# Kernel optimization log

Measured on AMD Instinct MI355X. Metric: run time of the kernel, lower is better.

## Reference

```python
import jax, jax.numpy as jnp
import numpy as np

NL, H, PD, NH, NB = 4, 256, 64, 4, 65
B, L, AA = 2, 384, 48
DH = H // NH
MAX_REL = 32


def _ln(x, g, b):
    m = x.mean(-1, keepdims=True)
    v = ((x - m) ** 2).mean(-1, keepdims=True)
    return (x - m) * jax.lax.rsqrt(v + 1e-5) * g + b


def setup_inputs() -> dict:
    key = jax.random.key(0)
    ks = iter(jax.random.split(key, 64))
    w = lambda *s: jax.random.normal(next(ks), s, jnp.float32) * 0.02
    return dict(
        x=jax.random.normal(next(ks), (B, L, AA), jnp.float32),
        rp_w=w(AA, H), rp_b=jnp.zeros((H,), jnp.float32),
        pos_embed=w(L, H),
        pii_w=w(H, PD), pii_b=jnp.zeros((PD,), jnp.float32),
        pij_w=w(H, PD), pij_b=jnp.zeros((PD,), jnp.float32),
        rel_emb=w(2 * MAX_REL + 2, PD),
        ln_seq_g=jnp.ones((NL, H), jnp.float32), ln_seq_b=jnp.zeros((NL, H), jnp.float32),
        ln_pair_g=jnp.ones((NL, PD), jnp.float32), ln_pair_b=jnp.zeros((NL, PD), jnp.float32),
        pb_w=w(NL, PD, NH),
        in_w=w(NL, H, 3 * H), in_b=jnp.zeros((NL, 3 * H), jnp.float32),
        out_w=w(NL, H, H), out_b=jnp.zeros((NL, H), jnp.float32),
        ff_ln_g=jnp.ones((NL, H), jnp.float32), ff_ln_b=jnp.zeros((NL, H), jnp.float32),
        ff_w1=w(NL, H, 4 * H), ff_b1=jnp.zeros((NL, 4 * H), jnp.float32),
        ff_w2=w(NL, 4 * H, H), ff_b2=jnp.zeros((NL, H), jnp.float32),
        pu_ln_g=jnp.ones((NL, PD), jnp.float32), pu_ln_b=jnp.zeros((NL, PD), jnp.float32),
        pu_w1=w(NL, PD, PD), pu_b1=jnp.zeros((NL, PD), jnp.float32),
        pu_w2=w(NL, PD, PD), pu_b2=jnp.zeros((NL, PD), jnp.float32),
        outer_w=w(NL, 2 * H, PD), outer_b=jnp.zeros((NL, PD), jnp.float32),
        dh_ln_g=jnp.ones((PD,), jnp.float32), dh_ln_b=jnp.zeros((PD,), jnp.float32),
        dh_w1=w(PD, PD), dh_b1=jnp.zeros((PD,), jnp.float32),
        dh_w2=w(PD, NB), dh_b2=jnp.zeros((NB,), jnp.float32),
    )


def reference(x, rp_w, rp_b, pos_embed, pii_w, pii_b, pij_w, pij_b, rel_emb,
              ln_seq_g, ln_seq_b, ln_pair_g, ln_pair_b, pb_w, in_w, in_b,
              out_w, out_b, ff_ln_g, ff_ln_b, ff_w1, ff_b1, ff_w2, ff_b2,
              pu_ln_g, pu_ln_b, pu_w1, pu_b1, pu_w2, pu_b2, outer_w, outer_b,
              dh_ln_g, dh_ln_b, dh_w1, dh_b1, dh_w2, dh_b2):
    Bx, Lx, _ = x.shape
    gelu = lambda t: jax.nn.gelu(t, approximate=False)  # torch nn.GELU default (erf)
    h = x @ rp_w + rp_b + pos_embed[:Lx][None]
    # pair init: outer sum of two linear projections + clipped rel-pos embedding
    pair = (h @ pii_w + pii_b)[:, :, None, :] + (h @ pij_w + pij_b)[:, None, :, :]
    idx = jnp.arange(Lx)
    rel = jnp.clip(idx[None, :] - idx[:, None], -MAX_REL, MAX_REL) + MAX_REL  # (L,L)
    pair = pair + rel_emb[rel][None]
    for i in range(NL):
        seq_n = _ln(h, ln_seq_g[i], ln_seq_b[i])
        bias = _ln(pair, ln_pair_g[i], ln_pair_b[i]) @ pb_w[i]  # (B,L,L,NH)
        mask = bias.mean(axis=(0, 3))  # torch: permute->reshape(B*NH,L,L)->mean(0)
        qkv = seq_n @ in_w[i] + in_b[i]
        q, k, v = jnp.split(qkv, 3, axis=-1)
        q = q.reshape(Bx, Lx, NH, DH)
        k = k.reshape(Bx, Lx, NH, DH)
        v = v.reshape(Bx, Lx, NH, DH)
        scores = jnp.einsum('blhd,bmhd->bhlm', q, k) / float(np.sqrt(DH)) + mask
        attn = jax.nn.softmax(scores, axis=-1)
        o = jnp.einsum('bhlm,bmhd->blhd', attn, v).reshape(Bx, Lx, H)
        h = h + o @ out_w[i] + out_b[i]
        h = h + gelu(_ln(h, ff_ln_g[i], ff_ln_b[i]) @ ff_w1[i] + ff_b1[i]) @ ff_w2[i] + ff_b2[i]
        # outer_proj(cat([h_i, h_j])) == h@W[:H] outer-summed with h@W[H:]
        oi = h @ outer_w[i][:H]
        oj = h @ outer_w[i][H:]
        outer = oi[:, :, None, :] + oj[:, None, :, :] + outer_b[i]  # (B,L,L,PD)
        pair = pair + gelu(_ln(outer, pu_ln_g[i], pu_ln_b[i]) @ pu_w1[i] + pu_b1[i]) @ pu_w2[i] + pu_b2[i]
    logits = gelu(_ln(pair, dh_ln_g, dh_ln_b) @ dh_w1 + dh_b1) @ dh_w2 + dh_b2
    return (logits + jnp.swapaxes(logits, 1, 2)) / 2.0
```

## Files before the change

### kernel.cpp

```cpp
#include <hip/hip_runtime.h>
#include <math.h>

#define LSEQ 384
#define HD 256
#define PDIM 64
#define NHEAD 4
#define NBINS 65
#define BATCH 2
#define NTT (LSEQ / 16)
#define NTRI (NTT * (NTT + 1) / 2)

typedef __attribute__((ext_vector_type(8))) short bf16x8;
typedef __attribute__((ext_vector_type(16))) float f32x16;
#define MFMA32(a, b, c) __builtin_amdgcn_mfma_f32_32x32x16_bf16(a, b, c, 0, 0, 0)

template<int CTRL, int RMASK>
__device__ __forceinline__ float dpp_sum_step(float v) {
    int x = __builtin_amdgcn_update_dpp(0, __float_as_int(v), CTRL, RMASK, 0xf, true);
    return v + __int_as_float(x);
}
template<int CTRL, int RMASK>
__device__ __forceinline__ float dpp_max_step(float v) {
    int x = __builtin_amdgcn_update_dpp(__float_as_int(v), __float_as_int(v), CTRL, RMASK, 0xf, false);
    return fmaxf(v, __int_as_float(x));
}
__device__ __forceinline__ float wsum(float v) {
    v = dpp_sum_step<0x111, 0xf>(v);
    v = dpp_sum_step<0x112, 0xf>(v);
    v = dpp_sum_step<0x114, 0xf>(v);
    v = dpp_sum_step<0x118, 0xf>(v);
    v = dpp_sum_step<0x142, 0xa>(v);
    v = dpp_sum_step<0x143, 0xc>(v);
    return __int_as_float(__builtin_amdgcn_readlane(__float_as_int(v), 63));
}
__device__ __forceinline__ float wmax(float v) {
    v = dpp_max_step<0x111, 0xf>(v);
    v = dpp_max_step<0x112, 0xf>(v);
    v = dpp_max_step<0x114, 0xf>(v);
    v = dpp_max_step<0x118, 0xf>(v);
    v = dpp_max_step<0x142, 0xa>(v);
    v = dpp_max_step<0x143, 0xc>(v);
    return __int_as_float(__builtin_amdgcn_readlane(__float_as_int(v), 63));
}
__device__ __forceinline__ float gelu_erf(float x) {
    return 0.5f * x * (1.0f + erff(x * 0.70710678f));
}

__device__ __forceinline__ unsigned short f2bf(float x) {
    unsigned u = __float_as_uint(x);
    unsigned r = (u + 0x7fff + ((u >> 16) & 1)) >> 16;
    return (unsigned short)r;
}
__device__ __forceinline__ float bf2f(unsigned short h) {
    return __uint_as_float(((unsigned)h) << 16);
}
__device__ __forceinline__ void split_bf(float x, unsigned short& h, unsigned short& l) {
    h = f2bf(x);
    l = f2bf(x - bf2f(h));
}

__global__ void k_h_init(const float* __restrict__ x, const float* __restrict__ rp_w,
                         const float* __restrict__ rp_b, const float* __restrict__ pos,
                         float* __restrict__ h) {
    __shared__ float xs[48];
    int row = blockIdx.x;
    int l = row % LSEQ;
    int t = threadIdx.x;
    if (t < 48) xs[t] = x[row * 48 + t];
    __syncthreads();
    float acc = rp_b[t] + pos[l * HD + t];
#pragma unroll 8
    for (int a = 0; a < 48; ++a) acc += xs[a] * rp_w[a * HD + t];
    h[row * HD + t] = acc;
}

__global__ void k_proj2(const float* __restrict__ h, const float* __restrict__ wA,
                        const float* __restrict__ wB, const float* __restrict__ bA,
                        const float* __restrict__ bB, int center,
                        float* __restrict__ pA, float* __restrict__ pB) {
    __shared__ float hs[HD];
    int row = blockIdx.x;
    int t = threadIdx.x;
    hs[t] = h[row * HD + t];
    hs[t + 128] = h[row * HD + t + 128];
    __syncthreads();
    int col = t & 63;
    const float* w = (t < 64) ? wA : wB;
    const float* bias = (t < 64) ? bA : bB;
    float acc = bias ? bias[col] : 0.0f;
#pragma unroll 8
    for (int a = 0; a < HD; ++a) acc += hs[a] * w[a * PDIM + col];
    if (center) {
        float mean = wsum(acc) * (1.0f / PDIM);
        acc -= mean;
    }
    float* p = (t < 64) ? pA : pB;
    p[row * PDIM + col] = acc;
}

__global__ void __launch_bounds__(64) k_pair_init2(
    const float* __restrict__ pi, const float* __restrict__ pj,
    const float* __restrict__ rel_emb, const float* __restrict__ gpb,
    const float* __restrict__ cbv, float* __restrict__ pair,
    float* __restrict__ mask_out) {
    __shared__ __align__(16) float pt[32][65];
    int blk = blockIdx.x;
    int row = blk / 12, seg = blk % 12;
    int b = row / LSEQ, i = row % LSEQ;
    int t = threadIdx.x;
    int pl = t & 31, hq = t >> 5;
    int j0 = seg * 32;
    float piv = pi[row * 64 + t];
    const float* pjb = pj + ((size_t)b * LSEQ + j0) * 64;
#pragma unroll 8
    for (int j = 0; j < 32; ++j) {
        int r = j0 + j - i; r = r < -32 ? -32 : (r > 32 ? 32 : r); r += 32;
        pt[j][t] = piv + pjb[j * 64 + t] + rel_emb[r * 64 + t];
    }
    __syncthreads();
    float4* dst4 = (float4*)(pair + ((size_t)row * LSEQ + j0) * 64);
    for (int n = t; n < 512; n += 64) {
        int r2 = n >> 4, c4 = (n & 15) << 2;
        float4 g4 = { pt[r2][c4], pt[r2][c4 + 1], pt[r2][c4 + 2], pt[r2][c4 + 3] };
        dst4[n] = g4;
    }
    float vv[32];
    float sv = 0.0f;
#pragma unroll
    for (int c = 0; c < 32; ++c) { vv[c] = pt[pl][hq * 32 + c]; sv += vv[c]; }
    sv += __shfl_xor(sv, 32);
    float mean = sv * (1.0f / PDIM);
    float sd2 = 0.0f, sdg = 0.0f;
#pragma unroll
    for (int c = 0; c < 32; ++c) {
        float d = vv[c] - mean;
        sd2 = fmaf(d, d, sd2);
        sdg = fmaf(d, gpb[hq * 32 + c], sdg);
    }
    sd2 += __shfl_xor(sd2, 32);
    sdg += __shfl_xor(sdg, 32);
    float rsv = rsqrtf(sd2 * (1.0f / PDIM) + 1e-5f);
    float dot = rsv * sdg + cbv[0];
    if (hq == 0)
        atomicAdd(mask_out + i * LSEQ + j0 + pl, dot * (1.0f / (BATCH * NHEAD)));
}

__global__ void k_prep(const float* __restrict__ pu_ln_g, const float* __restrict__ pu_ln_b,
                       const float* __restrict__ pu_w1, const float* __restrict__ pu_b1,
                       const float* __restrict__ pu_w2,
                       const float* __restrict__ dh_ln_g, const float* __restrict__ dh_ln_b,
                       const float* __restrict__ dh_w1, const float* __restrict__ dh_b1,
                       const float* __restrict__ dh_w2,
                       unsigned short* __restrict__ w1hT, unsigned short* __restrict__ w1lT,
                       unsigned short* __restrict__ w2hT, unsigned short* __restrict__ w2lT,
                       float* __restrict__ b1p, float* __restrict__ w2c) {
    int i = blockIdx.x;
    int c = threadIdx.x;
    const float *g, *bb, *w1, *b1, *w2;
    int w2s;
    if (i < 4) { g = pu_ln_g + i * 64; bb = pu_ln_b + i * 64; w1 = pu_w1 + i * 4096;
                 b1 = pu_b1 + i * 64; w2 = pu_w2 + i * 4096; w2s = 64; }
    else       { g = dh_ln_g; bb = dh_ln_b; w1 = dh_w1; b1 = dh_b1; w2 = dh_w2; w2s = 65; }
    float accb = b1[c];
    for (int k = 0; k < 64; ++k) {
        float wv = w1[k * 64 + c];
        accb += bb[k] * wv;
        unsigned short h, l;
        split_bf(g[k] * wv, h, l);
        w1hT[i * 4096 + c * 64 + k] = h;
        w1lT[i * 4096 + c * 64 + k] = l;
        split_bf(w2[k * w2s + c], h, l);
        w2hT[i * 4096 + c * 64 + k] = h;
        w2lT[i * 4096 + c * 64 + k] = l;
    }
    b1p[i * 64 + c] = accb;
    if (i == 4) w2c[c] = dh_w2[c * 65 + 64];
}

__global__ void k_maskprep(const float* __restrict__ g, const float* __restrict__ bb,
                           const float* __restrict__ pbw, float* __restrict__ gp,
                           float* __restrict__ cb) {
    int li = blockIdx.x;
    int c = threadIdx.x;
    const float* pw = pbw + li * PDIM * NHEAD;
    float pbs = pw[c * 4] + pw[c * 4 + 1] + pw[c * 4 + 2] + pw[c * 4 + 3];
    gp[li * 64 + c] = g[li * 64 + c] * pbs;
    float s = wsum(bb[li * 64 + c] * pbs);
    if (c == 0) cb[li] = s;
}

__global__ void k_split_T(const float* __restrict__ src, unsigned short* __restrict__ dh,
                          unsigned short* __restrict__ dl, int K, int N,
                          int tiles_k, int tiles_n, size_t sstride, size_t dstride) {
    __shared__ float lds[64][65];
    int bid = blockIdx.x;
    int tpl = tiles_k * tiles_n;
    int layer = bid / tpl;
    int rest = bid % tpl;
    int kt = rest / tiles_n, nt = rest % tiles_n;
    const float* s = src + layer * sstride;
    int t = threadIdx.x, c = t & 63, r0 = t >> 6;
    for (int r = r0; r < 64; r += 4)
        lds[r][c] = s[(size_t)(kt * 64 + r) * N + nt * 64 + c];
    __syncthreads();
    unsigned short* oh = dh + layer * dstride;
    unsigned short* ol = dl + layer * dstride;
    for (int r = r0; r < 64; r += 4) {
        float v = lds[c][r];
        unsigned short h, l;
        split_bf(v, h, l);
        size_t o = (size_t)(nt * 64 + r) * K + kt * 64 + c;
        oh[o] = h;
        ol[o] = l;
    }
}

template<bool GELU>
__global__ void __launch_bounds__(256) k_gemm(
    const float* __restrict__ X, const unsigned short* __restrict__ wTh,
    const unsigned short* __restrict__ wTl, const float* __restrict__ bias,
    const float* __restrict__ R, float* __restrict__ OUT, int K, int N) {
    int idx = blockIdx.x * 4 + (threadIdx.x >> 6);
    int lane = threadIdx.x & 63;
    int pl = lane & 31, hq = lane >> 5;
    int ntiles = N >> 5;
    int mt = idx / ntiles, nt = idx % ntiles;
    const float* xr = X + (size_t)(mt * 32 + pl) * K + 8 * hq;
    const unsigned short* bh = wTh + (size_t)(nt * 32 + pl) * K + 8 * hq;
    const unsigned short* bl = wTl + (size_t)(nt * 32 + pl) * K + 8 * hq;
    int n = nt * 32 + pl;
    float bv = bias[n];
    f32x16 acc;
#pragma unroll
    for (int r = 0; r < 16; ++r) {
        int mr = mt * 32 + (r & 3) + 8 * (r >> 2) + 4 * hq;
        acc[r] = bv + (R ? R[(size_t)mr * N + n] : 0.0f);
    }
#pragma unroll 4
    for (int s = 0; s < K; s += 16) {
        bf16x8 ah, al;
#pragma unroll
        for (int j = 0; j < 8; ++j) {
            unsigned short h, l;
            split_bf(xr[s + j], h, l);
            ah[j] = (short)h; al[j] = (short)l;
        }
        bf16x8 bhv = *(const bf16x8*)(bh + s);
        bf16x8 blv = *(const bf16x8*)(bl + s);
        acc = MFMA32(ah, bhv, acc);
        acc = MFMA32(al, bhv, acc);
        acc = MFMA32(ah, blv, acc);
    }
#pragma unroll
    for (int r = 0; r < 16; ++r) {
        int mr = mt * 32 + (r & 3) + 8 * (r >> 2) + 4 * hq;
        float v = acc[r];
        OUT[(size_t)mr * N + n] = GELU ? gelu_erf(v) : v;
    }
}

__global__ void k_ln_seq(const float* __restrict__ h, const float* __restrict__ g,
                         const float* __restrict__ b, float* __restrict__ out) {
    __shared__ float red[8];
    int row = blockIdx.x;
    int t = threadIdx.x;
    int w = t >> 6, lane = t & 63;
    float v = h[row * HD + t];
    float s = wsum(v);
    if (lane == 0) red[w] = s;
    __syncthreads();
    float mean = (red[0] + red[1] + red[2] + red[3]) * (1.0f / HD);
    float d = v - mean;
    float q = wsum(d * d);
    if (lane == 0) red[4 + w] = q;
    __syncthreads();
    float var = (red[4] + red[5] + red[6] + red[7]) * (1.0f / HD);
    out[row * HD + t] = d * rsqrtf(var + 1e-5f) * g[t] + b[t];
}

__global__ void k_attn(const float* __restrict__ qkv, const float* __restrict__ mask,
                       float* __restrict__ o) {
    __shared__ __align__(16) float qs[64];
    __shared__ float sc[LSEQ];
    __shared__ float red[8];
    __shared__ float op[4][64];
    int bid = blockIdx.x;
    int l = bid % LSEQ;
    int nh = (bid / LSEQ) & 3;
    int b = bid / (LSEQ * NHEAD);
    int t = threadIdx.x;
    int w = t >> 6, lane = t & 63;
    const float* qbase = qkv + ((size_t)(b * LSEQ + l)) * 768 + nh * 64;
    if (t < 64) qs[t] = qbase[t];
    __syncthreads();
    float lmax = -1e30f;
    float myv[2];
#pragma unroll
    for (int it = 0; it < 2; ++it) {
        int m = t + it * 256;
        if (m < LSEQ) {
            const float* kb = qkv + ((size_t)(b * LSEQ + m)) * 768 + 256 + nh * 64;
            const float4* k4 = (const float4*)kb;
            const float4* q4 = (const float4*)qs;
            float acc = 0.0f;
#pragma unroll
            for (int a = 0; a < 16; ++a) {
                float4 kv = k4[a], qv = q4[a];
                acc += qv.x * kv.x + qv.y * kv.y + qv.z * kv.z + qv.w * kv.w;
            }
            float s = acc * 0.125f + mask[l * LSEQ + m];
            myv[it] = s;
            lmax = fmaxf(lmax, s);
        } else myv[it] = -1e30f;
    }
    float wm = wmax(lmax);
    if (lane == 0) red[w] = wm;
    __syncthreads();
    float gmax = fmaxf(fmaxf(red[0], red[1]), fmaxf(red[2], red[3]));
    float lsum = 0.0f;
#pragma unroll
    for (int it = 0; it < 2; ++it) {
        int m = t + it * 256;
        if (m < LSEQ) {
            float e = expf(myv[it] - gmax);
            sc[m] = e;
            lsum += e;
        }
    }
    float ws = wsum(lsum);
    if (lane == 0) red[4 + w] = ws;
    __syncthreads();
    float inv = 1.0f / (red[4] + red[5] + red[6] + red[7]);
    int d = t & 63, gq = t >> 6;
    float part = 0.0f;
    for (int m = gq * 96; m < (gq + 1) * 96; ++m)
        part += sc[m] * qkv[((size_t)(b * LSEQ + m)) * 768 + 512 + nh * 64 + d];
    op[gq][d] = part;
    __syncthreads();
    if (t < 64) {
        float ov = (op[0][t] + op[1][t] + op[2][t] + op[3][t]) * inv;
        o[((size_t)(b * LSEQ + l)) * HD + nh * 64 + t] = ov;
    }
}

template<bool DIST>
__global__ void __launch_bounds__(64) k_pair_upd(
    const float* __restrict__ ojc,
    const float* __restrict__ oic,
    const unsigned short* __restrict__ w1hT, const unsigned short* __restrict__ w1lT,
    const float* __restrict__ b1p,
    const unsigned short* __restrict__ w2hT, const unsigned short* __restrict__ w2lT,
    const float* __restrict__ b2, float* __restrict__ pair,
    const float* __restrict__ gpb, const float* __restrict__ cbv,
    float* __restrict__ mask_out,
    const unsigned short* __restrict__ dw1h, const unsigned short* __restrict__ dw1l,
    const float* __restrict__ db1p,
    const unsigned short* __restrict__ dw2h, const unsigned short* __restrict__ dw2l,
    const float* __restrict__ w2c, const float* __restrict__ db2,
    float* __restrict__ outg) {
    __shared__ __align__(16) float pt[32][65];
    int blk = blockIdx.x;
    int row = blk / 12, seg = blk % 12;
    int b = row / LSEQ;
    int t = threadIdx.x;
    int pl = t & 31, hq = t >> 5;
    int p = seg * 32 + pl;
    const float* ojr = ojc + ((size_t)b * LSEQ + p) * 64;
    const float* oir = oic + (size_t)row * 64;
    float* prblk = pair + ((size_t)row * LSEQ + seg * 32) * 64;

    const float4* src4 = (const float4*)prblk;
    for (int n = t; n < 512; n += 64) {
        float4 g4 = src4[n];
        int r2 = n >> 4, ch = (n & 15) << 2;
        pt[r2][ch] = g4.x; pt[r2][ch + 1] = g4.y;
        pt[r2][ch + 2] = g4.z; pt[r2][ch + 3] = g4.w;
    }

    float v[32];
#pragma unroll
    for (int s = 0; s < 4; ++s) {
        int k0 = 16 * s + 8 * hq;
#pragma unroll
        for (int j = 0; j < 8; ++j) v[8 * s + j] = ojr[k0 + j] + oir[k0 + j];
    }
    float ss = 0.0f;
#pragma unroll
    for (int i = 0; i < 32; ++i) ss = fmaf(v[i], v[i], ss);
    ss += __shfl_xor(ss, 32);
    float rs = rsqrtf(ss * (1.0f / PDIM) + 1e-5f);
    bf16x8 zh[4], zl[4];
#pragma unroll
    for (int s = 0; s < 4; ++s)
#pragma unroll
        for (int j = 0; j < 8; ++j) {
            unsigned short h, l;
            split_bf(v[8 * s + j] * rs, h, l);
            zh[s][j] = (short)h; zl[s][j] = (short)l;
        }

    f32x16 acc0, acc1;
#pragma unroll
    for (int r = 0; r < 16; ++r) {
        int rr = (r & 3) + 8 * (r >> 2) + 4 * hq;
        acc0[r] = b1p[rr];
        acc1[r] = b1p[32 + rr];
    }
#pragma unroll
    for (int s = 0; s < 4; ++s) {
        int ko = 16 * s + 8 * hq;
        bf16x8 a0h = *(const bf16x8*)(w1hT + (pl << 6) + ko);
        bf16x8 a0l = *(const bf16x8*)(w1lT + (pl << 6) + ko);
        bf16x8 a1h = *(const bf16x8*)(w1hT + ((32 + pl) << 6) + ko);
        bf16x8 a1l = *(const bf16x8*)(w1lT + ((32 + pl) << 6) + ko);
        acc0 = MFMA32(a0h, zh[s], acc0);
        acc0 = MFMA32(a0h, zl[s], acc0);
        acc0 = MFMA32(a0l, zh[s], acc0);
        acc1 = MFMA32(a1h, zh[s], acc1);
        acc1 = MFMA32(a1h, zl[s], acc1);
        acc1 = MFMA32(a1l, zh[s], acc1);
    }
    float u0[16], u1[16];
#pragma unroll
    for (int r = 0; r < 16; ++r) { u0[r] = gelu_erf(acc0[r]); u1[r] = gelu_erf(acc1[r]); }

    float rA0[4], rB0[4], rA1[4], rB1[4];
#pragma unroll
    for (int i = 0; i < 4; ++i) {
        rA0[i] = __shfl_xor(hq ? u0[i] : u0[4 + i], 32);
        rB0[i] = __shfl_xor(hq ? u0[8 + i] : u0[12 + i], 32);
        rA1[i] = __shfl_xor(hq ? u1[i] : u1[4 + i], 32);
        rB1[i] = __shfl_xor(hq ? u1[8 + i] : u1[12 + i], 32);
    }
    bf16x8 uh[4], ul[4];
#pragma unroll
    for (int s = 0; s < 4; ++s) {
        int tt = s >> 1, q = s & 1;
#pragma unroll
        for (int i = 0; i < 4; ++i) {
            float own_f = q ? (tt ? u1[8 + i] : u0[8 + i]) : (tt ? u1[i] : u0[i]);
            float own_s = q ? (tt ? u1[12 + i] : u0[12 + i]) : (tt ? u1[4 + i] : u0[4 + i]);
            float rcv   = q ? (tt ? rB1[i] : rB0[i]) : (tt ? rA1[i] : rA0[i]);
            float f  = hq ? rcv : own_f;
            float g2 = hq ? own_s : rcv;
            unsigned short h, l;
            split_bf(f, h, l);  uh[s][i] = (short)h;     ul[s][i] = (short)l;
            split_bf(g2, h, l); uh[s][4 + i] = (short)h; ul[s][4 + i] = (short)l;
        }
    }

    __syncthreads();
    f32x16 c0, c1;
#pragma unroll
    for (int r = 0; r < 16; ++r) {
        int rr = (r & 3) + 8 * (r >> 2) + 4 * hq;
        c0[r] = b2[rr] + pt[pl][rr];
        c1[r] = b2[32 + rr] + pt[pl][32 + rr];
    }
#pragma unroll
    for (int s = 0; s < 4; ++s) {
        int ko = 16 * s + 8 * hq;
        bf16x8 a0h = *(const bf16x8*)(w2hT + (pl << 6) + ko);
        bf16x8 a0l = *(const bf16x8*)(w2lT + (pl << 6) + ko);
        bf16x8 a1h = *(const bf16x8*)(w2hT + ((32 + pl) << 6) + ko);
        bf16x8 a1l = *(const bf16x8*)(w2lT + ((32 + pl) << 6) + ko);
        c0 = MFMA32(a0h, uh[s], c0);
        c0 = MFMA32(a0h, ul[s], c0);
        c0 = MFMA32(a0l, uh[s], c0);
        c1 = MFMA32(a1h, uh[s], c1);
        c1 = MFMA32(a1h, ul[s], c1);
        c1 = MFMA32(a1l, uh[s], c1);
    }

    if constexpr (!DIST) {
#pragma unroll
        for (int r = 0; r < 16; ++r) {
            int rr = (r & 3) + 8 * (r >> 2) + 4 * hq;
            pt[pl][rr] = c0[r];
            pt[pl][32 + rr] = c1[r];
        }
        if (mask_out) {
            float sv = 0.0f;
#pragma unroll
            for (int r = 0; r < 16; ++r) sv += c0[r] + c1[r];
            sv += __shfl_xor(sv, 32);
            float mean = sv * (1.0f / PDIM);
            float sd2 = 0.0f, sdg = 0.0f;
#pragma unroll 4
            for (int r = 0; r < 16; ++r) {
                int rr = (r & 3) + 8 * (r >> 2) + 4 * hq;
                float d0 = c0[r] - mean, d1 = c1[r] - mean;
                sd2 = fmaf(d0, d0, sd2);
                sd2 = fmaf(d1, d1, sd2);
                sdg = fmaf(d0, gpb[rr], sdg);
                sdg = fmaf(d1, gpb[32 + rr], sdg);
            }
            sd2 += __shfl_xor(sd2, 32);
            sdg += __shfl_xor(sdg, 32);
            float rsv = rsqrtf(sd2 * (1.0f / PDIM) + 1e-5f);
            float dot = rsv * sdg + cbv[0];
            if (hq == 0)
                atomicAdd(mask_out + (row % LSEQ) * LSEQ + p, dot * (1.0f / (BATCH * NHEAD)));
        }
        __syncthreads();
        float4* dst4 = (float4*)prblk;
        for (int n = t; n < 512; n += 64) {
            int r2 = n >> 4, ch = (n & 15) << 2;
            float4 g4 = { pt[r2][ch], pt[r2][ch + 1], pt[r2][ch + 2], pt[r2][ch + 3] };
            dst4[n] = g4;
        }
    } else {
#pragma unroll
        for (int r = 0; r < 16; ++r) {
            int rr = (r & 3) + 8 * (r >> 2) + 4 * hq;
            pt[pl][rr] = c0[r];
            pt[pl][32 + rr] = c1[r];
        }
        __syncthreads();
        float v2[32];
#pragma unroll
        for (int s = 0; s < 4; ++s) {
            int k0 = 16 * s + 8 * hq;
#pragma unroll
            for (int j = 0; j < 8; ++j) v2[8 * s + j] = pt[pl][k0 + j];
        }
        float sm = 0.0f;
#pragma unroll
        for (int i = 0; i < 32; ++i) sm += v2[i];
        sm += __shfl_xor(sm, 32);
        float mean = sm * (1.0f / PDIM);
        float ss2 = 0.0f;
#pragma unroll
        for (int i = 0; i < 32; ++i) { v2[i] -= mean; ss2 = fmaf(v2[i], v2[i], ss2); }
        ss2 += __shfl_xor(ss2, 32);
        float rs2 = rsqrtf(ss2 * (1.0f / PDIM) + 1e-5f);
#pragma unroll
        for (int s = 0; s < 4; ++s)
#pragma unroll
            for (int j = 0; j < 8; ++j) {
                unsigned short h, l;
                split_bf(v2[8 * s + j] * rs2, h, l);
                zh[s][j] = (short)h; zl[s][j] = (short)l;
            }
#pragma unroll
        for (int r = 0; r < 16; ++r) {
            int rr = (r & 3) + 8 * (r >> 2) + 4 * hq;
            acc0[r] = db1p[rr];
            acc1[r] = db1p[32 + rr];
        }
#pragma unroll
        for (int s = 0; s < 4; ++s) {
            int ko = 16 * s + 8 * hq;
            bf16x8 a0h = *(const bf16x8*)(dw1h + (pl << 6) + ko);
            bf16x8 a0l = *(const bf16x8*)(dw1l + (pl << 6) + ko);
            bf16x8 a1h = *(const bf16x8*)(dw1h + ((32 + pl) << 6) + ko);
            bf16x8 a1l = *(const bf16x8*)(dw1l + ((32 + pl) << 6) + ko);
            acc0 = MFMA32(a0h, zh[s], acc0);
            acc0 = MFMA32(a0h, zl[s], acc0);
            acc0 = MFMA32(a0l, zh[s], acc0);
            acc1 = MFMA32(a1h, zh[s], acc1);
            acc1 = MFMA32(a1h, zl[s], acc1);
            acc1 = MFMA32(a1l, zh[s], acc1);
        }
        float p64 = 0.0f;
#pragma unroll
        for (int r = 0; r < 16; ++r) {
            int rr = (r & 3) + 8 * (r >> 2) + 4 * hq;
            u0[r] = gelu_erf(acc0[r]);
            u1[r] = gelu_erf(acc1[r]);
            p64 = fmaf(u0[r], w2c[rr], p64);
            p64 = fmaf(u1[r], w2c[32 + rr], p64);
        }
        p64 += __shfl_xor(p64, 32);
#pragma unroll
        for (int i = 0; i < 4; ++i) {
            rA0[i] = __shfl_xor(hq ? u0[i] : u0[4 + i], 32);
            rB0[i] = __shfl_xor(hq ? u0[8 + i] : u0[12 + i], 32);
            rA1[i] = __shfl_xor(hq ? u1[i] : u1[4 + i], 32);
            rB1[i] = __shfl_xor(hq ? u1[8 + i] : u1[12 + i], 32);
        }
#pragma unroll
        for (int s = 0; s < 4; ++s) {
            int tt = s >> 1, q = s & 1;
#pragma unroll
            for (int i = 0; i < 4; ++i) {
                float own_f = q ? (tt ? u1[8 + i] : u0[8 + i]) : (tt ? u1[i] : u0[i]);
                float own_s = q ? (tt ? u1[12 + i] : u0[12 + i]) : (tt ? u1[4 + i] : u0[4 + i]);
                float rcv   = q ? (tt ? rB1[i] : rB0[i]) : (tt ? rA1[i] : rA0[i]);
                float f  = hq ? rcv : own_f;
                float g2 = hq ? own_s : rcv;
                unsigned short h, l;
                split_bf(f, h, l);  uh[s][i] = (short)h;     ul[s][i] = (short)l;
                split_bf(g2, h, l); uh[s][4 + i] = (short)h; ul[s][4 + i] = (short)l;
            }
        }
#pragma unroll
        for (int r = 0; r < 16; ++r) {
            int rr = (r & 3) + 8 * (r >> 2) + 4 * hq;
            c0[r] = db2[rr];
            c1[r] = db2[32 + rr];
        }
#pragma unroll
        for (int s = 0; s < 4; ++s) {
            int ko = 16 * s + 8 * hq;
            bf16x8 a0h = *(const bf16x8*)(dw2h + (pl << 6) + ko);
            bf16x8 a0l = *(const bf16x8*)(dw2l + (pl << 6) + ko);
            bf16x8 a1h = *(const bf16x8*)(dw2h + ((32 + pl) << 6) + ko);
            bf16x8 a1l = *(const bf16x8*)(dw2l + ((32 + pl) << 6) + ko);
            c0 = MFMA32(a0h, uh[s], c0);
            c0 = MFMA32(a0h, ul[s], c0);
            c0 = MFMA32(a0l, uh[s], c0);
            c1 = MFMA32(a1h, uh[s], c1);
            c1 = MFMA32(a1h, ul[s], c1);
            c1 = MFMA32(a1l, uh[s], c1);
        }
        __syncthreads();
#pragma unroll
        for (int r = 0; r < 16; ++r) {
            int rr = (r & 3) + 8 * (r >> 2) + 4 * hq;
            pt[pl][rr] = c0[r];
            pt[pl][32 + rr] = c1[r];
        }
        if (hq == 0) pt[pl][64] = p64 + db2[64];
        __syncthreads();
        float4* dst = (float4*)(outg + ((size_t)row * LSEQ + seg * 32) * NBINS);
        const float4* srcl = (const float4*)&pt[0][0];
        for (int n = t; n < 520; n += 64) dst[n] = srcl[n];
    }
}

__global__ void k_sym(float* __restrict__ out) {
    int u = blockIdx.x;
    int b = 0;
    if (u >= NTRI) { b = 1; u -= NTRI; }
    int lt = 0, rem = NTT;
    while (u >= rem) { u -= rem; ++lt; --rem; }
    int mt = lt + u;
    int t = threadIdx.x;
    int g = t >> 6, lane = t & 63;
    float* ob = out + (size_t)b * LSEQ * LSEQ * NBINS;
    for (int e = g; e < 256; e += 4) {
        int i = e >> 4, j = e & 15;
        if (lt == mt && j < i) continue;
        size_t ia = ((size_t)(lt * 16 + i) * LSEQ + (mt * 16 + j)) * NBINS;
        size_t ib = ((size_t)(mt * 16 + j) * LSEQ + (lt * 16 + i)) * NBINS;
        for (int k = lane; k < NBINS; k += 64) {
            float a = ob[ia + k], c = ob[ib + k];
            float vv = 0.5f * (a + c);
            ob[ia + k] = vv;
            if (ia != ib) ob[ib + k] = vv;
        }
    }
}

extern "C" void kernel_launch(void* const* d_in, const int* in_sizes, int n_in,
                              void* d_out, int out_size, void* d_ws, size_t ws_size,
                              hipStream_t stream) {
    const float* x        = (const float*)d_in[0];
    const float* rp_w     = (const float*)d_in[1];
    const float* rp_b     = (const float*)d_in[2];
    const float* pos      = (const float*)d_in[3];
    const float* pii_w    = (const float*)d_in[4];
    const float* pii_b    = (const float*)d_in[5];
    const float* pij_w    = (const float*)d_in[6];
    const float* pij_b    = (const float*)d_in[7];
    const float* rel_emb  = (const float*)d_in[8];
    const float* ln_seq_g = (const float*)d_in[9];
    const float* ln_seq_b = (const float*)d_in[10];
    const float* ln_pair_g= (const float*)d_in[11];
    const float* ln_pair_b= (const float*)d_in[12];
    const float* pb_w     = (const float*)d_in[13];
    const float* in_w     = (const float*)d_in[14];
    const float* in_b     = (const float*)d_in[15];
    const float* out_w    = (const float*)d_in[16];
    const float* out_b    = (const float*)d_in[17];
    const float* ff_ln_g  = (const float*)d_in[18];
    const float* ff_ln_b  = (const float*)d_in[19];
    const float* ff_w1    = (const float*)d_in[20];
    const float* ff_b1    = (const float*)d_in[21];
    const float* ff_w2    = (const float*)d_in[22];
    const float* ff_b2    = (const float*)d_in[23];
    const float* pu_ln_g  = (const float*)d_in[24];
    const float* pu_ln_b  = (const float*)d_in[25];
    const float* pu_w1    = (const float*)d_in[26];
    const float* pu_b1    = (const float*)d_in[27];
    const float* pu_w2    = (const float*)d_in[28];
    const float* pu_b2    = (const float*)d_in[29];
    const float* outer_w  = (const float*)d_in[30];
    const float* outer_b  = (const float*)d_in[31];
    const float* dh_ln_g  = (const float*)d_in[32];
    const float* dh_ln_b  = (const float*)d_in[33];
    const float* dh_w1    = (const float*)d_in[34];
    const float* dh_b1    = (const float*)d_in[35];
    const float* dh_w2    = (const float*)d_in[36];
    const float* dh_b2    = (const float*)d_in[37];
    float* outp = (float*)d_out;

    float* W = (float*)d_ws;
    float* h    = W;  W += BATCH * LSEQ * HD;
    float* sn   = W;  W += BATCH * LSEQ * HD;
    float* qkv  = W;  W += BATCH * LSEQ * 3 * HD;
    float* ob   = W;  W += BATCH * LSEQ * HD;
    float* mid  = W;  W += BATCH * LSEQ * 4 * HD;
    float* maskA= W;  W += LSEQ * LSEQ;
    float* maskB= W;  W += LSEQ * LSEQ;
    float* poi  = W;  W += BATCH * LSEQ * PDIM;
    float* poj  = W;  W += BATCH * LSEQ * PDIM;
    float* b1p  = W;  W += 5 * 64;
    float* w2c  = W;  W += 64;
    float* gpb  = W;  W += 4 * 64;
    float* cbv  = W;  W += 64;
    unsigned short* w1hT = (unsigned short*)W;  W += 5 * 2048;
    unsigned short* w1lT = (unsigned short*)W;  W += 5 * 2048;
    unsigned short* w2hT = (unsigned short*)W;  W += 5 * 2048;
    unsigned short* w2lT = (unsigned short*)W;  W += 5 * 2048;
    unsigned short* qwT_h = (unsigned short*)W;  W += 4 * 196608 / 2;
    unsigned short* qwT_l = (unsigned short*)W;  W += 4 * 196608 / 2;
    unsigned short* owT_h = (unsigned short*)W;  W += 4 * 65536 / 2;
    unsigned short* owT_l = (unsigned short*)W;  W += 4 * 65536 / 2;
    unsigned short* f1T_h = (unsigned short*)W;  W += 4 * 262144 / 2;
    unsigned short* f1T_l = (unsigned short*)W;  W += 4 * 262144 / 2;
    unsigned short* f2T_h = (unsigned short*)W;  W += 4 * 262144 / 2;
    unsigned short* f2T_l = (unsigned short*)W;  W += 4 * 262144 / 2;
    float* pair = W;  W += (size_t)BATCH * LSEQ * LSEQ * PDIM;

    const int rows = BATCH * LSEQ;

    k_prep<<<5, 64, 0, stream>>>(pu_ln_g, pu_ln_b, pu_w1, pu_b1, pu_w2,
                                 dh_ln_g, dh_ln_b, dh_w1, dh_b1, dh_w2,
                                 w1hT, w1lT, w2hT, w2lT, b1p, w2c);
    k_maskprep<<<4, 64, 0, stream>>>(ln_pair_g, ln_pair_b, pb_w, gpb, cbv);
    k_split_T<<<4 * 4 * 12, 256, 0, stream>>>(in_w,  qwT_h, qwT_l, 256, 768,  4, 12, 196608, 196608);
    k_split_T<<<4 * 4 * 4,  256, 0, stream>>>(out_w, owT_h, owT_l, 256, 256,  4, 4,  65536,  65536);
    k_split_T<<<4 * 4 * 16, 256, 0, stream>>>(ff_w1, f1T_h, f1T_l, 256, 1024, 4, 16, 262144, 262144);
    k_split_T<<<4 * 16 * 4, 256, 0, stream>>>(ff_w2, f2T_h, f2T_l, 1024, 256, 16, 4, 262144, 262144);
    k_h_init<<<rows, 256, 0, stream>>>(x, rp_w, rp_b, pos, h);
    k_proj2<<<rows, 128, 0, stream>>>(h, pii_w, pij_w, pii_b, pij_b, 0, poi, poj);
    hipMemsetAsync(maskA, 0, LSEQ * LSEQ * sizeof(float), stream);
    k_pair_init2<<<rows * 12, 64, 0, stream>>>(poi, poj, rel_emb, gpb, cbv, pair, maskA);

    float* mcur = maskA;
    float* mnext = maskB;
    for (int i = 0; i < 4; ++i) {
        k_ln_seq<<<rows, 256, 0, stream>>>(h, ln_seq_g + i * HD, ln_seq_b + i * HD, sn);
        k_gemm<false><<<144, 256, 0, stream>>>(sn, qwT_h + i * 196608, qwT_l + i * 196608,
                                               in_b + i * 768, nullptr, qkv, 256, 768);
        k_attn<<<BATCH * NHEAD * LSEQ, 256, 0, stream>>>(qkv, mcur, ob);
        k_gemm<false><<<48, 256, 0, stream>>>(ob, owT_h + i * 65536, owT_l + i * 65536,
                                              out_b + i * 256, h, h, 256, 256);
        k_ln_seq<<<rows, 256, 0, stream>>>(h, ff_ln_g + i * HD, ff_ln_b + i * HD, sn);
        k_gemm<true><<<192, 256, 0, stream>>>(sn, f1T_h + i * 262144, f1T_l + i * 262144,
                                              ff_b1 + i * 1024, nullptr, mid, 256, 1024);
        k_gemm<false><<<48, 256, 0, stream>>>(mid, f2T_h + i * 262144, f2T_l + i * 262144,
                                              ff_b2 + i * 256, h, h, 1024, 256);
        k_proj2<<<rows, 128, 0, stream>>>(h, outer_w + i * 2 * HD * PDIM,
                                          outer_w + i * 2 * HD * PDIM + HD * PDIM,
                                          outer_b + i * PDIM, nullptr, 1, poi, poj);
        if (i < 3) {
            hipMemsetAsync(mnext, 0, LSEQ * LSEQ * sizeof(float), stream);
            k_pair_upd<false><<<rows * 12, 64, 0, stream>>>(
                poj, poi,
                w1hT + i * 4096, w1lT + i * 4096, b1p + i * 64,
                w2hT + i * 4096, w2lT + i * 4096, pu_b2 + i * PDIM, pair,
                gpb + (i + 1) * 64, cbv + (i + 1), mnext,
                nullptr, nullptr, nullptr, nullptr, nullptr, nullptr, nullptr, nullptr);
            float* tmp = mcur; mcur = mnext; mnext = tmp;
        } else {
            k_pair_upd<true><<<rows * 12, 64, 0, stream>>>(
                poj, poi,
                w1hT + 3 * 4096, w1lT + 3 * 4096, b1p + 3 * 64,
                w2hT + 3 * 4096, w2lT + 3 * 4096, pu_b2 + 3 * PDIM, pair,
                nullptr, nullptr, nullptr,
                w1hT + 4 * 4096, w1lT + 4 * 4096, b1p + 4 * 64,
                w2hT + 4 * 4096, w2lT + 4 * 4096, w2c, dh_b2, outp);
        }
    }

    k_sym<<<2 * NTRI, 256, 0, stream>>>(outp);
}
```

Before: 1.168 ms.

## Stage pair-update weights in LDS with 4-wave blocks and packed bf16 conversion

The pair-update kernel moves from one-wave blocks of 32 pairs to four-wave blocks of 128 pairs. It stages the hi/lo bf16 weight matrices in shared memory once per block instead of each wave reading them from global memory. Pair rows are now read and written directly in MFMA register layout with vector loads, which removes the LDS transpose round-trip and one barrier. The hi/lo bf16 split now uses the packed v_cvt_pk_bf16_f32 instruction in both the pair kernel and the GEMM, and the GEMM loads its activations as float4. The larger blocks use more LDS, especially in the distance-head variant, which may lower occupancy.

```diff
diff --git a/kernel.cpp b/kernel.cpp
--- a/kernel.cpp
+++ b/kernel.cpp
@@ -12,6 +12,9 @@
 
 typedef __attribute__((ext_vector_type(8))) short bf16x8;
 typedef __attribute__((ext_vector_type(16))) float f32x16;
+typedef __attribute__((ext_vector_type(4))) float f32x4;
+typedef __attribute__((ext_vector_type(4))) unsigned u32x4;
+typedef __attribute__((ext_vector_type(4))) short s16x4;
 #define MFMA32(a, b, c) __builtin_amdgcn_mfma_f32_32x32x16_bf16(a, b, c, 0, 0, 0)
 
 template<int CTRL, int RMASK>
@@ -57,6 +60,34 @@
 __device__ __forceinline__ void split_bf(float x, unsigned short& h, unsigned short& l) {
     h = f2bf(x);
     l = f2bf(x - bf2f(h));
+}
+
+__device__ __forceinline__ unsigned cvt_pk_bf(float lo, float hi) {
+    unsigned r;
+    asm("v_cvt_pk_bf16_f32 %0, %1, %2" : "=v"(r) : "v"(lo), "v"(hi));
+    return r;
+}
+__device__ __forceinline__ void pack8(const float* v, u32x4& h, u32x4& l) {
+#pragma unroll
+    for (int j = 0; j < 4; ++j) {
+        float a = v[2 * j], b = v[2 * j + 1];
+        unsigned hp = cvt_pk_bf(a, b);
+        float ra = a - __uint_as_float(hp << 16);
+        float rb = b - __uint_as_float(hp & 0xffff0000u);
+        h[j] = hp;
+        l[j] = cvt_pk_bf(ra, rb);
+    }
+}
+__device__ __forceinline__ bf16x8 as_bf(u32x4 x) {
+    union { u32x4 u; bf16x8 b; } c; c.u = x; return c.b;
+}
+__device__ __forceinline__ bf16x8 ld8(const short* p) {
+    s16x4 a = *(const s16x4*)p;
+    s16x4 b = *(const s16x4*)(p + 4);
+    bf16x8 r;
+    r[0] = a[0]; r[1] = a[1]; r[2] = a[2]; r[3] = a[3];
+    r[4] = b[0]; r[5] = b[1]; r[6] = b[2]; r[7] = b[3];
+    return r;
 }
 
 __global__ void k_h_init(const float* __restrict__ x, const float* __restrict__ rp_w,
@@ -238,18 +269,18 @@
     }
 #pragma unroll 4
     for (int s = 0; s < K; s += 16) {
-        bf16x8 ah, al;
-#pragma unroll
-        for (int j = 0; j < 8; ++j) {
-            unsigned short h, l;
-            split_bf(xr[s + j], h, l);
-            ah[j] = (short)h; al[j] = (short)l;
-        }
+        const f32x4* x4 = (const f32x4*)(xr + s);
+        f32x4 xa = x4[0], xb = x4[1];
+        float xv[8];
+#pragma unroll
+        for (int j = 0; j < 4; ++j) { xv[j] = xa[j]; xv[4 + j] = xb[j]; }
+        u32x4 ah, al;
+        pack8(xv, ah, al);
         bf16x8 bhv = *(const bf16x8*)(bh + s);
         bf16x8 blv = *(const bf16x8*)(bl + s);
-        acc = MFMA32(ah, bhv, acc);
-        acc = MFMA32(al, bhv, acc);
-        acc = MFMA32(ah, blv, acc);
+        acc = MFMA32(as_bf(ah), bhv, acc);
+        acc = MFMA32(as_bf(al), bhv, acc);
+        acc = MFMA32(as_bf(ah), blv, acc);
     }
 #pragma unroll
     for (int r = 0; r < 16; ++r) {
@@ -344,7 +375,7 @@
 }
 
 template<bool DIST>
-__global__ void __launch_bounds__(64) k_pair_upd(
+__global__ void __launch_bounds__(256) k_pair_upd(
     const float* __restrict__ ojc,
     const float* __restrict__ oic,
     const unsigned short* __restrict__ w1hT, const unsigned short* __restrict__ w1lT,
@@ -358,71 +389,101 @@
     const unsigned short* __restrict__ dw2h, const unsigned short* __restrict__ dw2l,
     const float* __restrict__ w2c, const float* __restrict__ db2,
     float* __restrict__ outg) {
-    __shared__ __align__(16) float pt[32][65];
+    __shared__ short lw[4][64][68];
+    constexpr int PTR = DIST ? 128 : 1;
+    __shared__ __align__(16) float pt[PTR][65];
     int blk = blockIdx.x;
-    int row = blk / 12, seg = blk % 12;
+    int row = blk / 3, seg = blk % 3;
     int b = row / LSEQ;
     int t = threadIdx.x;
-    int pl = t & 31, hq = t >> 5;
-    int p = seg * 32 + pl;
+    int wave = t >> 6, lane = t & 63;
+    int pl = lane & 31, hq = lane >> 5;
+    int jj = wave * 32 + pl;
+    int p = seg * 128 + jj;
     const float* ojr = ojc + ((size_t)b * LSEQ + p) * 64;
     const float* oir = oic + (size_t)row * 64;
-    float* prblk = pair + ((size_t)row * LSEQ + seg * 32) * 64;
-
-    const float4* src4 = (const float4*)prblk;
-    for (int n = t; n < 512; n += 64) {
-        float4 g4 = src4[n];
-        int r2 = n >> 4, ch = (n & 15) << 2;
-        pt[r2][ch] = g4.x; pt[r2][ch + 1] = g4.y;
-        pt[r2][ch + 2] = g4.z; pt[r2][ch + 3] = g4.w;
-    }
+    float* prp = pair + ((size_t)row * LSEQ + p) * 64;
 
     float v[32];
-#pragma unroll
-    for (int s = 0; s < 4; ++s) {
-        int k0 = 16 * s + 8 * hq;
-#pragma unroll
-        for (int j = 0; j < 8; ++j) v[8 * s + j] = ojr[k0 + j] + oir[k0 + j];
-    }
+    {
+        const f32x4* a4 = (const f32x4*)ojr;
+        const f32x4* c4 = (const f32x4*)oir;
+#pragma unroll
+        for (int s = 0; s < 4; ++s) {
+            f32x4 a = a4[4 * s + 2 * hq], aa = a4[4 * s + 2 * hq + 1];
+            f32x4 c = c4[4 * s + 2 * hq], cc = c4[4 * s + 2 * hq + 1];
+#pragma unroll
+            for (int j = 0; j < 4; ++j) {
+                v[8 * s + j] = a[j] + c[j];
+                v[8 * s + 4 + j] = aa[j] + cc[j];
+            }
+        }
+    }
+#define STAGE_W(a2, src) \
+    for (int idx = t; idx < 2048; idx += 256) { \
+        int rr2 = idx >> 5, cc2 = idx & 31; \
+        *(unsigned*)(&lw[a2][rr2][cc2 * 2]) = *(const unsigned*)(src + rr2 * 64 + cc2 * 2); \
+    }
+    STAGE_W(0, w1hT)
+    STAGE_W(1, w1lT)
+    STAGE_W(2, w2hT)
+    STAGE_W(3, w2lT)
+
     float ss = 0.0f;
 #pragma unroll
     for (int i = 0; i < 32; ++i) ss = fmaf(v[i], v[i], ss);
     ss += __shfl_xor(ss, 32);
     float rs = rsqrtf(ss * (1.0f / PDIM) + 1e-5f);
-    bf16x8 zh[4], zl[4];
-#pragma unroll
-    for (int s = 0; s < 4; ++s)
-#pragma unroll
-        for (int j = 0; j < 8; ++j) {
-            unsigned short h, l;
-            split_bf(v[8 * s + j] * rs, h, l);
-            zh[s][j] = (short)h; zl[s][j] = (short)l;
-        }
+#pragma unroll
+    for (int i = 0; i < 32; ++i) v[i] *= rs;
+    u32x4 zh[4], zl[4];
+#pragma unroll
+    for (int s = 0; s < 4; ++s) pack8(v + 8 * s, zh[s], zl[s]);
+
+    const f32x4* b14 = (const f32x4*)b1p;
+    f32x4 bi0[4], bi1[4];
+#pragma unroll
+    for (int g = 0; g < 4; ++g) { bi0[g] = b14[2 * g + hq]; bi1[g] = b14[8 + 2 * g + hq]; }
+
+    __syncthreads();
 
     f32x16 acc0, acc1;
 #pragma unroll
     for (int r = 0; r < 16; ++r) {
-        int rr = (r & 3) + 8 * (r >> 2) + 4 * hq;
-        acc0[r] = b1p[rr];
-        acc1[r] = b1p[32 + rr];
+        acc0[r] = bi0[r >> 2][r & 3];
+        acc1[r] = bi1[r >> 2][r & 3];
     }
 #pragma unroll
     for (int s = 0; s < 4; ++s) {
         int ko = 16 * s + 8 * hq;
-        bf16x8 a0h = *(const bf16x8*)(w1hT + (pl << 6) + ko);
-        bf16x8 a0l = *(const bf16x8*)(w1lT + (pl << 6) + ko);
-        bf16x8 a1h = *(const bf16x8*)(w1hT + ((32 + pl) << 6) + ko);
-        bf16x8 a1l = *(const bf16x8*)(w1lT + ((32 + pl) << 6) + ko);
-        acc0 = MFMA32(a0h, zh[s], acc0);
-        acc0 = MFMA32(a0h, zl[s], acc0);
-        acc0 = MFMA32(a0l, zh[s], acc0);
-        acc1 = MFMA32(a1h, zh[s], acc1);
-        acc1 = MFMA32(a1h, zl[s], acc1);
-        acc1 = MFMA32(a1l, zh[s], acc1);
+        bf16x8 a0h = ld8(&lw[0][pl][ko]);
+        bf16x8 a0l = ld8(&lw[1][pl][ko]);
+        bf16x8 a1h = ld8(&lw[0][32 + pl][ko]);
+        bf16x8 a1l = ld8(&lw[1][32 + pl][ko]);
+        bf16x8 zhs = as_bf(zh[s]), zls = as_bf(zl[s]);
+        acc0 = MFMA32(a0h, zhs, acc0);
+        acc0 = MFMA32(a0h, zls, acc0);
+        acc0 = MFMA32(a0l, zhs, acc0);
+        acc1 = MFMA32(a1h, zhs, acc1);
+        acc1 = MFMA32(a1h, zls, acc1);
+        acc1 = MFMA32(a1l, zhs, acc1);
     }
     float u0[16], u1[16];
 #pragma unroll
     for (int r = 0; r < 16; ++r) { u0[r] = gelu_erf(acc0[r]); u1[r] = gelu_erf(acc1[r]); }
+
+    f32x4 r0[4], r1[4], q0[4], q1[4];
+    {
+        const f32x4* pr4 = (const f32x4*)prp;
+        const f32x4* b24 = (const f32x4*)b2;
+#pragma unroll
+        for (int g = 0; g < 4; ++g) {
+            r0[g] = pr4[2 * g + hq];
+            r1[g] = pr4[8 + 2 * g + hq];
+            q0[g] = b24[2 * g + hq];
+            q1[g] = b24[8 + 2 * g + hq];
+        }
+    }
 
     float rA0[4], rB0[4], rA1[4], rB1[4];
 #pragma unroll
@@ -432,97 +493,93 @@
         rA1[i] = __shfl_xor(hq ? u1[i] : u1[4 + i], 32);
         rB1[i] = __shfl_xor(hq ? u1[8 + i] : u1[12 + i], 32);
     }
-    bf16x8 uh[4], ul[4];
+    u32x4 uh[4], ul[4];
 #pragma unroll
     for (int s = 0; s < 4; ++s) {
         int tt = s >> 1, q = s & 1;
+        float fg[8];
 #pragma unroll
         for (int i = 0; i < 4; ++i) {
             float own_f = q ? (tt ? u1[8 + i] : u0[8 + i]) : (tt ? u1[i] : u0[i]);
             float own_s = q ? (tt ? u1[12 + i] : u0[12 + i]) : (tt ? u1[4 + i] : u0[4 + i]);
             float rcv   = q ? (tt ? rB1[i] : rB0[i]) : (tt ? rA1[i] : rA0[i]);
-            float f  = hq ? rcv : own_f;
-            float g2 = hq ? own_s : rcv;
-            unsigned short h, l;
-            split_bf(f, h, l);  uh[s][i] = (short)h;     ul[s][i] = (short)l;
-            split_bf(g2, h, l); uh[s][4 + i] = (short)h; ul[s][4 + i] = (short)l;
-        }
-    }
-
-    __syncthreads();
+            fg[i]     = hq ? rcv : own_f;
+            fg[4 + i] = hq ? own_s : rcv;
+        }
+        pack8(fg, uh[s], ul[s]);
+    }
+
     f32x16 c0, c1;
 #pragma unroll
     for (int r = 0; r < 16; ++r) {
-        int rr = (r & 3) + 8 * (r >> 2) + 4 * hq;
-        c0[r] = b2[rr] + pt[pl][rr];
-        c1[r] = b2[32 + rr] + pt[pl][32 + rr];
+        int g = r >> 2, i = r & 3;
+        c0[r] = q0[g][i] + r0[g][i];
+        c1[r] = q1[g][i] + r1[g][i];
     }
 #pragma unroll
     for (int s = 0; s < 4; ++s) {
         int ko = 16 * s + 8 * hq;
-        bf16x8 a0h = *(const bf16x8*)(w2hT + (pl << 6) + ko);
-        bf16x8 a0l = *(const bf16x8*)(w2lT + (pl << 6) + ko);
-        bf16x8 a1h = *(const bf16x8*)(w2hT + ((32 + pl) << 6) + ko);
-        bf16x8 a1l = *(const bf16x8*)(w2lT + ((32 + pl) << 6) + ko);
-        c0 = MFMA32(a0h, uh[s], c0);
-        c0 = MFMA32(a0h, ul[s], c0);
-        c0 = MFMA32(a0l, uh[s], c0);
-        c1 = MFMA32(a1h, uh[s], c1);
-        c1 = MFMA32(a1h, ul[s], c1);
-        c1 = MFMA32(a1l, uh[s], c1);
+        bf16x8 a0h = ld8(&lw[2][pl][ko]);
+        bf16x8 a0l = ld8(&lw[3][pl][ko]);
+        bf16x8 a1h = ld8(&lw[2][32 + pl][ko]);
+        bf16x8 a1l = ld8(&lw[3][32 + pl][ko]);
+        bf16x8 uhs = as_bf(uh[s]), uls = as_bf(ul[s]);
+        c0 = MFMA32(a0h, uhs, c0);
+        c0 = MFMA32(a0h, uls, c0);
+        c0 = MFMA32(a0l, uhs, c0);
+        c1 = MFMA32(a1h, uhs, c1);
+        c1 = MFMA32(a1h, uls, c1);
+        c1 = MFMA32(a1l, uhs, c1);
     }
 
     if constexpr (!DIST) {
+        const f32x4* gp4 = (const f32x4*)gpb;
+        f32x4 gp0[4], gp1[4];
+#pragma unroll
+        for (int g = 0; g < 4; ++g) { gp0[g] = gp4[2 * g + hq]; gp1[g] = gp4[8 + 2 * g + hq]; }
+        float sv = 0.0f;
+#pragma unroll
+        for (int r = 0; r < 16; ++r) sv += c0[r] + c1[r];
+        sv += __shfl_xor(sv, 32);
+        float mean = sv * (1.0f / PDIM);
+        float sd2 = 0.0f, sdg = 0.0f;
+#pragma unroll 4
+        for (int r = 0; r < 16; ++r) {
+            int g = r >> 2, i = r & 3;
+            float d0 = c0[r] - mean, d1 = c1[r] - mean;
+            sd2 = fmaf(d0, d0, sd2);
+            sd2 = fmaf(d1, d1, sd2);
+            sdg = fmaf(d0, gp0[g][i], sdg);
+            sdg = fmaf(d1, gp1[g][i], sdg);
+        }
+        sd2 += __shfl_xor(sd2, 32);
+        sdg += __shfl_xor(sdg, 32);
+        float rsv = rsqrtf(sd2 * (1.0f / PDIM) + 1e-5f);
+        float dot = rsv * sdg + cbv[0];
+        if (hq == 0)
+            atomicAdd(mask_out + (row % LSEQ) * LSEQ + p, dot * (1.0f / (BATCH * NHEAD)));
+        f32x4* pw4 = (f32x4*)prp;
+#pragma unroll
+        for (int g = 0; g < 4; ++g) {
+            f32x4 s0, s1;
+#pragma unroll
+            for (int i = 0; i < 4; ++i) { s0[i] = c0[4 * g + i]; s1[i] = c1[4 * g + i]; }
+            pw4[2 * g + hq] = s0;
+            pw4[8 + 2 * g + hq] = s1;
+        }
+    } else {
 #pragma unroll
         for (int r = 0; r < 16; ++r) {
             int rr = (r & 3) + 8 * (r >> 2) + 4 * hq;
-            pt[pl][rr] = c0[r];
-            pt[pl][32 + rr] = c1[r];
-        }
-        if (mask_out) {
-            float sv = 0.0f;
-#pragma unroll
-            for (int r = 0; r < 16; ++r) sv += c0[r] + c1[r];
-            sv += __shfl_xor(sv, 32);
-            float mean = sv * (1.0f / PDIM);
-            float sd2 = 0.0f, sdg = 0.0f;
-#pragma unroll 4
-            for (int r = 0; r < 16; ++r) {
-                int rr = (r & 3) + 8 * (r >> 2) + 4 * hq;
-                float d0 = c0[r] - mean, d1 = c1[r] - mean;
-                sd2 = fmaf(d0, d0, sd2);
-                sd2 = fmaf(d1, d1, sd2);
-                sdg = fmaf(d0, gpb[rr], sdg);
-                sdg = fmaf(d1, gpb[32 + rr], sdg);
-            }
-            sd2 += __shfl_xor(sd2, 32);
-            sdg += __shfl_xor(sdg, 32);
-            float rsv = rsqrtf(sd2 * (1.0f / PDIM) + 1e-5f);
-            float dot = rsv * sdg + cbv[0];
-            if (hq == 0)
-                atomicAdd(mask_out + (row % LSEQ) * LSEQ + p, dot * (1.0f / (BATCH * NHEAD)));
-        }
-        __syncthreads();
-        float4* dst4 = (float4*)prblk;
-        for (int n = t; n < 512; n += 64) {
-            int r2 = n >> 4, ch = (n & 15) << 2;
-            float4 g4 = { pt[r2][ch], pt[r2][ch + 1], pt[r2][ch + 2], pt[r2][ch + 3] };
-            dst4[n] = g4;
-        }
-    } else {
-#pragma unroll
-        for (int r = 0; r < 16; ++r) {
-            int rr = (r & 3) + 8 * (r >> 2) + 4 * hq;
-            pt[pl][rr] = c0[r];
-            pt[pl][32 + rr] = c1[r];
-        }
-        __syncthreads();
+            pt[jj][rr] = c0[r];
+            pt[jj][32 + rr] = c1[r];
+        }
         float v2[32];
 #pragma unroll
         for (int s = 0; s < 4; ++s) {
             int k0 = 16 * s + 8 * hq;
 #pragma unroll
-            for (int j = 0; j < 8; ++j) v2[8 * s + j] = pt[pl][k0 + j];
+            for (int j = 0; j < 8; ++j) v2[8 * s + j] = pt[jj][k0 + j];
         }
         float sm = 0.0f;
 #pragma unroll
@@ -535,41 +592,55 @@
         ss2 += __shfl_xor(ss2, 32);
         float rs2 = rsqrtf(ss2 * (1.0f / PDIM) + 1e-5f);
 #pragma unroll
-        for (int s = 0; s < 4; ++s)
-#pragma unroll
-            for (int j = 0; j < 8; ++j) {
-                unsigned short h, l;
-                split_bf(v2[8 * s + j] * rs2, h, l);
-                zh[s][j] = (short)h; zl[s][j] = (short)l;
-            }
+        for (int i = 0; i < 32; ++i) v2[i] *= rs2;
+#pragma unroll
+        for (int s = 0; s < 4; ++s) pack8(v2 + 8 * s, zh[s], zl[s]);
+
+        __syncthreads();
+        STAGE_W(0, dw1h)
+        STAGE_W(1, dw1l)
+        STAGE_W(2, dw2h)
+        STAGE_W(3, dw2l)
+        const f32x4* d14 = (const f32x4*)db1p;
+        const f32x4* d24 = (const f32x4*)db2;
+        const f32x4* wc4 = (const f32x4*)w2c;
+        f32x4 di0[4], di1[4], e0[4], e1[4], wc0[4], wc1[4];
+#pragma unroll
+        for (int g = 0; g < 4; ++g) {
+            di0[g] = d14[2 * g + hq]; di1[g] = d14[8 + 2 * g + hq];
+            e0[g] = d24[2 * g + hq];  e1[g] = d24[8 + 2 * g + hq];
+            wc0[g] = wc4[2 * g + hq]; wc1[g] = wc4[8 + 2 * g + hq];
+        }
+        __syncthreads();
+
 #pragma unroll
         for (int r = 0; r < 16; ++r) {
-            int rr = (r & 3) + 8 * (r >> 2) + 4 * hq;
-            acc0[r] = db1p[rr];
-            acc1[r] = db1p[32 + rr];
+            acc0[r] = di0[r >> 2][r & 3];
+            acc1[r] = di1[r >> 2][r & 3];
         }
 #pragma unroll
         for (int s = 0; s < 4; ++s) {
             int ko = 16 * s + 8 * hq;
-            bf16x8 a0h = *(const bf16x8*)(dw1h + (pl << 6) + ko);
-            bf16x8 a0l = *(const bf16x8*)(dw1l + (pl << 6) + ko);
-            bf16x8 a1h = *(const bf16x8*)(dw1h + ((32 + pl) << 6) + ko);
-            bf16x8 a1l = *(const bf16x8*)(dw1l + ((32 + pl) << 6) + ko);
-            acc0 = MFMA32(a0h, zh[s], acc0);
-            acc0 = MFMA32(a0h, zl[s], acc0);
-            acc0 = MFMA32(a0l, zh[s], acc0);
-            acc1 = MFMA32(a1h, zh[s], acc1);
-            acc1 = MFMA32(a1h, zl[s], acc1);
-            acc1 = MFMA32(a1l, zh[s], acc1);
+            bf16x8 a0h = ld8(&lw[0][pl][ko]);
+            bf16x8 a0l = ld8(&lw[1][pl][ko]);
+            bf16x8 a1h = ld8(&lw[0][32 + pl][ko]);
+            bf16x8 a1l = ld8(&lw[1][32 + pl][ko]);
+            bf16x8 zhs = as_bf(zh[s]), zls = as_bf(zl[s]);
+            acc0 = MFMA32(a0h, zhs, acc0);
+            acc0 = MFMA32(a0h, zls, acc0);
+            acc0 = MFMA32(a0l, zhs, acc0);
+            acc1 = MFMA32(a1h, zhs, acc1);
+            acc1 = MFMA32(a1h, zls, acc1);
+            acc1 = MFMA32(a1l, zhs, acc1);
         }
         float p64 = 0.0f;
 #pragma unroll
         for (int r = 0; r < 16; ++r) {
-            int rr = (r & 3) + 8 * (r >> 2) + 4 * hq;
+            int g = r >> 2, i = r & 3;
             u0[r] = gelu_erf(acc0[r]);
             u1[r] = gelu_erf(acc1[r]);
-            p64 = fmaf(u0[r], w2c[rr], p64);
-            p64 = fmaf(u1[r], w2c[32 + rr], p64);
+            p64 = fmaf(u0[r], wc0[g][i], p64);
+            p64 = fmaf(u1[r], wc1[g][i], p64);
         }
         p64 += __shfl_xor(p64, 32);
 #pragma unroll
@@ -582,51 +653,50 @@
 #pragma unroll
         for (int s = 0; s < 4; ++s) {
             int tt = s >> 1, q = s & 1;
+            float fg[8];
 #pragma unroll
             for (int i = 0; i < 4; ++i) {
                 float own_f = q ? (tt ? u1[8 + i] : u0[8 + i]) : (tt ? u1[i] : u0[i]);
                 float own_s = q ? (tt ? u1[12 + i] : u0[12 + i]) : (tt ? u1[4 + i] : u0[4 + i]);
                 float rcv   = q ? (tt ? rB1[i] : rB0[i]) : (tt ? rA1[i] : rA0[i]);
-                float f  = hq ? rcv : own_f;
-                float g2 = hq ? own_s : rcv;
-                unsigned short h, l;
-                split_bf(f, h, l);  uh[s][i] = (short)h;     ul[s][i] = (short)l;
-                split_bf(g2, h, l); uh[s][4 + i] = (short)h; ul[s][4 + i] = (short)l;
+                fg[i]     = hq ? rcv : own_f;
+                fg[4 + i] = hq ? own_s : rcv;
             }
+            pack8(fg, uh[s], ul[s]);
+        }
+#pragma unroll
+        for (int r = 0; r < 16; ++r) {
+            c0[r] = e0[r >> 2][r & 3];
+            c1[r] = e1[r >> 2][r & 3];
+        }
+#pragma unroll
+        for (int s = 0; s < 4; ++s) {
+            int ko = 16 * s + 8 * hq;
+            bf16x8 a0h = ld8(&lw[2][pl][ko]);
+            bf16x8 a0l = ld8(&lw[3][pl][ko]);
+            bf16x8 a1h = ld8(&lw[2][32 + pl][ko]);
+            bf16x8 a1l = ld8(&lw[3][32 + pl][ko]);
+            bf16x8 uhs = as_bf(uh[s]), uls = as_bf(ul[s]);
+            c0 = MFMA32(a0h, uhs, c0);
+            c0 = MFMA32(a0h, uls, c0);
+            c0 = MFMA32(a0l, uhs, c0);
+            c1 = MFMA32(a1h, uhs, c1);
+            c1 = MFMA32(a1h, uls, c1);
+            c1 = MFMA32(a1l, uhs, c1);
         }
 #pragma unroll
         for (int r = 0; r < 16; ++r) {
             int rr = (r & 3) + 8 * (r >> 2) + 4 * hq;
-            c0[r] = db2[rr];
-            c1[r] = db2[32 + rr];
-        }
-#pragma unroll
-        for (int s = 0; s < 4; ++s) {
-            int ko = 16 * s + 8 * hq;
-            bf16x8 a0h = *(const bf16x8*)(dw2h + (pl << 6) + ko);
-            bf16x8 a0l = *(const bf16x8*)(dw2l + (pl << 6) + ko);
-            bf16x8 a1h = *(const bf16x8*)(dw2h + ((32 + pl) << 6) + ko);
-            bf16x8 a1l = *(const bf16x8*)(dw2l + ((32 + pl) << 6) + ko);
-            c0 = MFMA32(a0h, uh[s], c0);
-            c0 = MFMA32(a0h, ul[s], c0);
-            c0 = MFMA32(a0l, uh[s], c0);
-            c1 = MFMA32(a1h, uh[s], c1);
-            c1 = MFMA32(a1h, ul[s], c1);
-            c1 = MFMA32(a1l, uh[s], c1);
-        }
+            pt[jj][rr] = c0[r];
+            pt[jj][32 + rr] = c1[r];
+        }
+        if (hq == 0) pt[jj][64] = p64 + db2[64];
         __syncthreads();
-#pragma unroll
-        for (int r = 0; r < 16; ++r) {
-            int rr = (r & 3) + 8 * (r >> 2) + 4 * hq;
-            pt[pl][rr] = c0[r];
-            pt[pl][32 + rr] = c1[r];
-        }
-        if (hq == 0) pt[pl][64] = p64 + db2[64];
-        __syncthreads();
-        float4* dst = (float4*)(outg + ((size_t)row * LSEQ + seg * 32) * NBINS);
+        float4* dst = (float4*)(outg + ((size_t)row * LSEQ + seg * 128) * NBINS);
         const float4* srcl = (const float4*)&pt[0][0];
-        for (int n = t; n < 520; n += 64) dst[n] = srcl[n];
-    }
+        for (int n = t; n < 128 * NBINS / 4; n += 256) dst[n] = srcl[n];
+    }
+#undef STAGE_W
 }
 
 __global__ void k_sym(float* __restrict__ out) {
@@ -758,7 +828,7 @@
                                           outer_b + i * PDIM, nullptr, 1, poi, poj);
         if (i < 3) {
             hipMemsetAsync(mnext, 0, LSEQ * LSEQ * sizeof(float), stream);
-            k_pair_upd<false><<<rows * 12, 64, 0, stream>>>(
+            k_pair_upd<false><<<rows * 3, 256, 0, stream>>>(
                 poj, poi,
                 w1hT + i * 4096, w1lT + i * 4096, b1p + i * 64,
                 w2hT + i * 4096, w2lT + i * 4096, pu_b2 + i * PDIM, pair,
@@ -766,7 +836,7 @@
                 nullptr, nullptr, nullptr, nullptr, nullptr, nullptr, nullptr, nullptr);
             float* tmp = mcur; mcur = mnext; mnext = tmp;
         } else {
-            k_pair_upd<true><<<rows * 12, 64, 0, stream>>>(
+            k_pair_upd<true><<<rows * 3, 256, 0, stream>>>(
                 poj, poi,
                 w1hT + 3 * 4096, w1lT + 3 * 4096, b1p + 3 * 64,
                 w2hT + 3 * 4096, w2lT + 3 * 4096, pu_b2 + 3 * PDIM, pair,
```

Measured after the change: 1.117 ms. 1.05x faster.
